# Optimization experiments

Measured on AMD Instinct MI355X. Metric: run time of the kernel, lower is better.

Reference implementation:

```python
import jax, jax.numpy as jnp
import numpy as np

N = 50000
E = 800000
IN_DIM = 128
EMB_DIM = 64
HID = 128
OUT_DIM = 64
VOCAB = 1000
NUM_GRAPHS = 128


def _gat(x, src, dst, W, a_s, a_d, b, n):
    # PyG GATConv, heads=1: h = x @ W (no bias); alpha_e = leaky_relu(a_s.h_src + a_d.h_dst, 0.2)
    h = x @ W                                  # [n, C]
    as_n = h @ a_s                             # [n]
    ad_n = h @ a_d                             # [n]
    logit = jax.nn.leaky_relu(as_n[src] + ad_n[dst], negative_slope=0.2)  # [E']
    # segment softmax over destination node
    m = jax.ops.segment_max(logit, dst, num_segments=n)
    e = jnp.exp(logit - m[dst])
    s = jax.ops.segment_sum(e, dst, num_segments=n)
    coef = e / s[dst]                          # [E']
    out = jax.ops.segment_sum(h[src] * coef[:, None], dst, num_segments=n)
    return out + b


def setup_inputs() -> dict:
    key = jax.random.key(0)
    ks = jax.random.split(key, 20)
    inp = {
        "x": jax.random.normal(ks[0], (N, IN_DIM), dtype=jnp.float32),
        "node_index": jax.random.randint(ks[1], (N,), 0, VOCAB),
        "edge_index": jax.random.randint(ks[2], (2, E), 0, N),
        "batch": jnp.sort(jax.random.randint(ks[3], (N,), 0, NUM_GRAPHS)),
        "emb": jax.random.normal(ks[4], (VOCAB, EMB_DIM), dtype=jnp.float32) * 0.1,
        "W1": jax.random.normal(ks[5], (IN_DIM + EMB_DIM, HID), dtype=jnp.float32) * 0.05,
        "a1s": jax.random.normal(ks[6], (HID,), dtype=jnp.float32) * 0.1,
        "a1d": jax.random.normal(ks[7], (HID,), dtype=jnp.float32) * 0.1,
        "b1": jnp.zeros((HID,), dtype=jnp.float32),
        "W2": jax.random.normal(ks[8], (HID, HID), dtype=jnp.float32) * 0.05,
        "a2s": jax.random.normal(ks[9], (HID,), dtype=jnp.float32) * 0.1,
        "a2d": jax.random.normal(ks[10], (HID,), dtype=jnp.float32) * 0.1,
        "b2": jnp.zeros((HID,), dtype=jnp.float32),
        "W3": jax.random.normal(ks[11], (HID, HID), dtype=jnp.float32) * 0.05,
        "a3s": jax.random.normal(ks[12], (HID,), dtype=jnp.float32) * 0.1,
        "a3d": jax.random.normal(ks[13], (HID,), dtype=jnp.float32) * 0.1,
        "b3": jnp.zeros((HID,), dtype=jnp.float32),
        "fcW": jax.random.normal(ks[14], (HID, OUT_DIM), dtype=jnp.float32) * 0.05,
        "fcb": jnp.zeros((OUT_DIM,), dtype=jnp.float32),
    }
    return inp


def reference(x, node_index, edge_index, batch, emb, W1, a1s, a1d, b1,
              W2, a2s, a2d, b2, W3, a3s, a3d, b3, fcW, fcb):
    n = x.shape[0]
    # embedding lookup + L2 normalize features, then concat
    ev = emb[node_index]                       # [N, EMB_DIM]
    norms = jnp.linalg.norm(x, axis=1, keepdims=True)
    norms = jnp.where(norms == 0, 1e-8, norms)
    h = jnp.concatenate([x / norms, ev], axis=1)  # [N, IN+EMB]
    # add self loops (PyG GATConv default add_self_loops=True)
    loop = jnp.arange(n)
    src = jnp.concatenate([edge_index[0], loop])
    dst = jnp.concatenate([edge_index[1], loop])
    h = jax.nn.gelu(_gat(h, src, dst, W1, a1s, a1d, b1, n))
    h = jax.nn.gelu(_gat(h, src, dst, W2, a2s, a2d, b2, n))
    h = jax.nn.gelu(_gat(h, src, dst, W3, a3s, a3d, b3, n))
    # global_add_pool over graphs
    g = jax.ops.segment_sum(h, batch, num_segments=NUM_GRAPHS)  # [G, HID]
    out = g @ fcW + fcb
    return jax.nn.leaky_relu(out, negative_slope=0.01)
```

## Files before the change

### kernel.cpp

```cpp
#include <hip/hip_runtime.h>

#define N_NODES 50000
#define N_EDGES 800000
#define IN_DIM 128
#define EMB_DIM 64
#define HID 128
#define OUT_DIM 64
#define NUM_GRAPHS 128
#define E_TOT (N_EDGES + N_NODES)
#define K1 (IN_DIM + EMB_DIM)
#define NB 391
#define EPT 16
#define EPB (256 * EPT)
#define PREPA_BLOCKS 12500
#define BHIST_BLOCKS 512

typedef __attribute__((ext_vector_type(8))) short bf16x8;
typedef __attribute__((ext_vector_type(4))) float f32x4;

__device__ __forceinline__ float gelu_f(float x) {
    float x3 = x * x * x;
    return 0.5f * x * (1.0f + tanhf(0.7978845608028654f * (x + 0.044715f * x3)));
}
__device__ __forceinline__ float lrelu02(float x) { return x > 0.f ? x : 0.2f * x; }
__device__ __forceinline__ float rl_f(float v, int j) {
    return __int_as_float(__builtin_amdgcn_readlane(__float_as_int(v), j));
}
__device__ __forceinline__ unsigned short f2bf(float f) {
    unsigned u = __float_as_uint(f);
    unsigned r = (u + 0x7fffu + ((u >> 16) & 1u)) >> 16;
    return (unsigned short)r;
}
__device__ __forceinline__ unsigned pk2bf(float a, float b) {
    return (unsigned)f2bf(a) | ((unsigned)f2bf(b) << 16);
}

__global__ __launch_bounds__(128) void k_prepW3(const float* __restrict__ W1, unsigned short* __restrict__ Wt1,
                                                const float* __restrict__ W2, unsigned short* __restrict__ Wt2,
                                                const float* __restrict__ W3, unsigned short* __restrict__ Wt3,
                                                int* __restrict__ bcnt, int* __restrict__ bfill) {
    int b = blockIdx.x;
    int c = threadIdx.x;
    if (b == K1 + 2 * HID) {
        for (int i = c; i < NB; i += 128) { bcnt[i] = 0; bfill[i] = 0; }
        return;
    }
    if (b < K1) {
        Wt1[(size_t)c * (K1 + 8) + b] = f2bf(W1[(size_t)b * HID + c]);
    } else if (b < K1 + HID) {
        int k = b - K1;
        Wt2[(size_t)c * (HID + 8) + k] = f2bf(W2[(size_t)k * HID + c]);
    } else {
        int k = b - K1 - HID;
        Wt3[(size_t)c * (HID + 8) + k] = f2bf(W3[(size_t)k * HID + c]);
    }
}

__global__ __launch_bounds__(256) void k_prepA_bhist(const float* __restrict__ x, const int* __restrict__ nidx,
                                                     const float* __restrict__ emb, unsigned* __restrict__ Abu,
                                                     const int* __restrict__ dst, int* __restrict__ bcnt) {
    __shared__ int h[NB];
    if (blockIdx.x >= PREPA_BLOCKS) {
        int nb = blockIdx.x - PREPA_BLOCKS;
        for (int i = threadIdx.x; i < NB; i += 256) h[i] = 0;
        __syncthreads();
        for (int e = nb * 256 + threadIdx.x; e < N_EDGES; e += BHIST_BLOCKS * 256)
            atomicAdd(&h[dst[e] >> 7], 1);
        __syncthreads();
        for (int i = threadIdx.x; i < NB; i += 256)
            if (h[i]) atomicAdd(&bcnt[i], h[i]);
        return;
    }
    int lane = threadIdx.x & 63;
    int node = (blockIdx.x * 256 + threadIdx.x) >> 6;
    if (node >= N_NODES) return;
    float2 v = ((const float2*)(x + (size_t)node * IN_DIM))[lane];
    float ss = v.x * v.x + v.y * v.y;
#pragma unroll
    for (int o = 32; o; o >>= 1) ss += __shfl_xor(ss, o);
    float nrm = sqrtf(ss);
    if (nrm == 0.f) nrm = 1e-8f;
    float inv = 1.f / nrm;
    unsigned* row = Abu + (size_t)node * (K1 / 2);
    row[lane] = pk2bf(v.x * inv, v.y * inv);
    int nid = __builtin_amdgcn_readfirstlane(nidx[node]);
    if (lane < 32) {
        float2 e = ((const float2*)(emb + (size_t)nid * EMB_DIM))[lane];
        row[64 + lane] = pk2bf(e.x, e.y);
    }
}

__global__ __launch_bounds__(512) void k_bscan(const int* __restrict__ bcnt, int* __restrict__ boff,
                                               int* __restrict__ rowptr) {
    __shared__ int sh[512];
    int t = threadIdx.x;
    int v = (t < NB) ? bcnt[t] : 0;
    sh[t] = v;
    __syncthreads();
    for (int o = 1; o < 512; o <<= 1) {
        int u = (t >= o) ? sh[t - o] : 0;
        __syncthreads();
        sh[t] += u;
        __syncthreads();
    }
    if (t < NB) boff[t] = sh[t] - v;
    if (t == NB - 1) boff[NB] = sh[t];
    if (t == 0) rowptr[N_NODES] = E_TOT;
}

__global__ __launch_bounds__(256) void k_passA(const int* __restrict__ src, const int* __restrict__ dst,
                                               const int* __restrict__ boff, int* __restrict__ bfill,
                                               unsigned* __restrict__ barr) {
    __shared__ int h[NB];
    __shared__ int base[NB];
    for (int i = threadIdx.x; i < NB; i += 256) h[i] = 0;
    __syncthreads();
    int e0 = blockIdx.x * EPB;
    int tag[EPT];
#pragma unroll
    for (int i = 0; i < EPT; i++) {
        int e = e0 + i * 256 + threadIdx.x;
        tag[i] = -1;
        if (e < N_EDGES) {
            int b = dst[e] >> 7;
            int r = atomicAdd(&h[b], 1);
            tag[i] = (b << 12) | r;
        }
    }
    __syncthreads();
    for (int i = threadIdx.x; i < NB; i += 256)
        base[i] = h[i] ? atomicAdd(&bfill[i], h[i]) : 0;
    __syncthreads();
#pragma unroll
    for (int i = 0; i < EPT; i++) {
        if (tag[i] >= 0) {
            int e = e0 + i * 256 + threadIdx.x;
            int b = tag[i] >> 12, r = tag[i] & 0xfff;
            unsigned s = (unsigned)src[e];
            unsigned dl = (unsigned)(dst[e] & 127);
            barr[boff[b] + base[b] + r] = s | (dl << 16);
        }
    }
}

__global__ __launch_bounds__(256) void k_passB(const unsigned* __restrict__ barr, const int* __restrict__ boff,
                                               int* __restrict__ rowptr, int* __restrict__ csr) {
    __shared__ int dcnt[128];
    __shared__ int dsum[128];
    __shared__ int locOff[128];
    int b = blockIdx.x;
    int t = threadIdx.x;
    int n0 = b << 7;
    int cnt = min(128, N_NODES - n0);
    int eb = boff[b], ee = boff[b + 1];
    if (t < 128) dcnt[t] = 0;
    __syncthreads();
    for (int i = eb + t; i < ee; i += 256) atomicAdd(&dcnt[barr[i] >> 16], 1);
    __syncthreads();
    int v = 0;
    if (t < 128) {
        v = (t < cnt) ? dcnt[t] + 1 : 0;
        dsum[t] = v;
    }
    __syncthreads();
    for (int o = 1; o < 128; o <<= 1) {
        int u = (t >= o && t < 128) ? dsum[t - o] : 0;
        __syncthreads();
        if (t < 128) dsum[t] += u;
        __syncthreads();
    }
    int csrBase = eb + n0;
    if (t < 128) {
        locOff[t] = dsum[t] - v;
        dcnt[t] = 0;
    }
    if (t < cnt) {
        int loc = dsum[t] - v;
        rowptr[n0 + t] = csrBase + loc;
        csr[csrBase + loc] = n0 + t;
    }
    __syncthreads();
    for (int i = eb + t; i < ee; i += 256) {
        unsigned vv = barr[i];
        int dl = vv >> 16;
        int s = (int)(vv & 0xffffu);
        int k = atomicAdd(&dcnt[dl], 1);
        csr[csrBase + locOff[dl] + 1 + k] = s;
    }
}

template <int K>
__global__ __launch_bounds__(256) void k_mgemm(const unsigned short* __restrict__ Abf,
                                               const unsigned short* __restrict__ WtP,
                                               const float* __restrict__ a_s, const float* __restrict__ a_d,
                                               unsigned short* __restrict__ Hbf,
                                               float* __restrict__ asn, float* __restrict__ adn) {
    constexpr int KP = K + 8;
    constexpr int NK = K / 32;
    __shared__ __align__(16) unsigned short Wl[128 * KP];
    {
        const uint4* gsrc = (const uint4*)WtP;
        uint4* ldst = (uint4*)Wl;
        const int nchunk = 128 * KP * 2 / 16;
        for (int i = threadIdx.x; i < nchunk; i += 256) ldst[i] = gsrc[i];
    }
    int lane = threadIdx.x & 63;
    int wv = threadIdx.x >> 6;
    int rowbase = blockIdx.x * 64 + wv * 16;
    if (rowbase >= N_NODES) { __syncthreads(); return; }
    int l15 = lane & 15, quad = lane >> 4;

    const unsigned short* Abase = Abf + (size_t)(rowbase + l15) * K + quad * 8;
    bf16x8 afr[NK];
#pragma unroll
    for (int i = 0; i < NK; i++) afr[i] = *(const bf16x8*)(Abase + i * 32);

    __syncthreads();

    f32x4 acc[8];
#pragma unroll
    for (int t = 0; t < 8; t++) acc[t] = (f32x4){0.f, 0.f, 0.f, 0.f};
#pragma unroll
    for (int i = 0; i < NK; i++) {
#pragma unroll
        for (int t = 0; t < 8; t++) {
            bf16x8 bf = *(const bf16x8*)(&Wl[(t * 16 + l15) * KP + i * 32 + quad * 8]);
            acc[t] = __builtin_amdgcn_mfma_f32_16x16x32_bf16(afr[i], bf, acc[t], 0, 0, 0);
        }
    }
    float asc[8], adc[8];
#pragma unroll
    for (int t = 0; t < 8; t++) { asc[t] = a_s[t * 16 + l15]; adc[t] = a_d[t * 16 + l15]; }
#pragma unroll
    for (int r = 0; r < 4; r++) {
        int row = rowbase + quad * 4 + r;
        float ps = 0.f, pd = 0.f;
#pragma unroll
        for (int t = 0; t < 8; t++) {
            float v = acc[t][r];
            Hbf[(size_t)row * HID + t * 16 + l15] = f2bf(v);
            ps = fmaf(v, asc[t], ps);
            pd = fmaf(v, adc[t], pd);
        }
#pragma unroll
        for (int o = 1; o < 16; o <<= 1) {
            ps += __shfl_xor(ps, o);
            pd += __shfl_xor(pd, o);
        }
        if (l15 == 0) { asn[row] = ps; adn[row] = pd; }
    }
}

template <bool OUT32>
__global__ __launch_bounds__(256) void k_aggr(const int* __restrict__ rowptr, const int* __restrict__ csr,
                                              const float* __restrict__ asn, const float* __restrict__ adn,
                                              const unsigned short* __restrict__ hbf,
                                              const float* __restrict__ bias, void* __restrict__ outp) {
    __shared__ float sh_e[4][64];
    __shared__ int sh_s[4][64];
    int lane = threadIdx.x & 63;
    int w = threadIdx.x >> 6;
    int node = blockIdx.x * 4 + w;
    if (node >= N_NODES) return;
    int st = rowptr[node], en = rowptr[node + 1];
    int deg = en - st;
    float ad = adn[node];

    if (deg <= 64) {
        int s = 0;
        float l = -1e30f;
        if (lane < deg) {
            s = csr[st + lane];
            l = lrelu02(asn[s] + ad);
        }
        float m = l;
#pragma unroll
        for (int o = 32; o; o >>= 1) m = fmaxf(m, __shfl_xor(m, o));
        float e = (lane < deg) ? __expf(l - m) : 0.f;
        float ssum = e;
#pragma unroll
        for (int o = 32; o; o >>= 1) ssum += __shfl_xor(ssum, o);
        float coef = e / ssum;

        const uint2* hu2 = (const uint2*)hbf;
        int half = lane >> 5, li = lane & 31;
        float4 acc = make_float4(0.f, 0.f, 0.f, 0.f);
        int j = 0;
        for (; j + 16 <= deg; j += 16) {
            int sx[8];
            float cf[8];
            uint2 vv[8];
#pragma unroll
            for (int q = 0; q < 8; q++) {
                int ii = j + 2 * q + half;
                sx[q] = __shfl(s, ii);
                cf[q] = __shfl(coef, ii);
            }
#pragma unroll
            for (int q = 0; q < 8; q++) vv[q] = hu2[(size_t)sx[q] * 32 + li];
#pragma unroll
            for (int q = 0; q < 8; q++) {
                acc.x = fmaf(cf[q], __int_as_float(vv[q].x << 16), acc.x);
                acc.y = fmaf(cf[q], __int_as_float(vv[q].x & 0xffff0000u), acc.y);
                acc.z = fmaf(cf[q], __int_as_float(vv[q].y << 16), acc.z);
                acc.w = fmaf(cf[q], __int_as_float(vv[q].y & 0xffff0000u), acc.w);
            }
        }
        for (; j + 8 <= deg; j += 8) {
            int sx[4];
            float cf[4];
            uint2 vv[4];
#pragma unroll
            for (int q = 0; q < 4; q++) {
                int ii = j + 2 * q + half;
                sx[q] = __shfl(s, ii);
                cf[q] = __shfl(coef, ii);
            }
#pragma unroll
            for (int q = 0; q < 4; q++) vv[q] = hu2[(size_t)sx[q] * 32 + li];
#pragma unroll
            for (int q = 0; q < 4; q++) {
                acc.x = fmaf(cf[q], __int_as_float(vv[q].x << 16), acc.x);
                acc.y = fmaf(cf[q], __int_as_float(vv[q].x & 0xffff0000u), acc.y);
                acc.z = fmaf(cf[q], __int_as_float(vv[q].y << 16), acc.z);
                acc.w = fmaf(cf[q], __int_as_float(vv[q].y & 0xffff0000u), acc.w);
            }
        }
        for (; j < deg; j += 2) {
            int ii = j + half;
            int ok = ii < deg;
            int ic = ok ? ii : j;
            int sx = __shfl(s, ic);
            float cf = __shfl(coef, ic);
            if (!ok) cf = 0.f;
            uint2 v = hu2[(size_t)sx * 32 + li];
            acc.x = fmaf(cf, __int_as_float(v.x << 16), acc.x);
            acc.y = fmaf(cf, __int_as_float(v.x & 0xffff0000u), acc.y);
            acc.z = fmaf(cf, __int_as_float(v.y << 16), acc.z);
            acc.w = fmaf(cf, __int_as_float(v.y & 0xffff0000u), acc.w);
        }
        acc.x += __shfl_xor(acc.x, 32);
        acc.y += __shfl_xor(acc.y, 32);
        acc.z += __shfl_xor(acc.z, 32);
        acc.w += __shfl_xor(acc.w, 32);
        float4 bb = ((const float4*)bias)[li];
        float r0 = gelu_f(acc.x + bb.x);
        float r1 = gelu_f(acc.y + bb.y);
        float r2 = gelu_f(acc.z + bb.z);
        float r3 = gelu_f(acc.w + bb.w);
        if (half == 0) {
            if constexpr (OUT32) {
                ((float4*)outp)[(size_t)node * 32 + li] = make_float4(r0, r1, r2, r3);
            } else {
                uint2 o;
                o.x = pk2bf(r0, r1);
                o.y = pk2bf(r2, r3);
                ((uint2*)outp)[(size_t)node * 32 + li] = o;
            }
        }
    } else {
        const unsigned* hu = (const unsigned*)hbf;
        float2 acc = make_float2(0.f, 0.f);
        float m = -1e30f;
        for (int i = st + lane; i < en; i += 64) {
            float l = lrelu02(asn[csr[i]] + ad);
            m = fmaxf(m, l);
        }
#pragma unroll
        for (int o = 32; o; o >>= 1) m = fmaxf(m, __shfl_xor(m, o));
        float ssum = 0.f;
        for (int i = st + lane; i < en; i += 64) {
            float l = lrelu02(asn[csr[i]] + ad);
            ssum += __expf(l - m);
        }
#pragma unroll
        for (int o = 32; o; o >>= 1) ssum += __shfl_xor(ssum, o);
        float inv = 1.f / ssum;
        for (int base = st; base < en; base += 64) {
            int cnt = min(64, en - base);
            if (lane < cnt) {
                int sx = csr[base + lane];
                float l = lrelu02(asn[sx] + ad);
                sh_e[w][lane] = __expf(l - m) * inv;
                sh_s[w][lane] = sx;
            }
            for (int j = 0; j < cnt; j++) {
                float c = sh_e[w][j];
                int sx = sh_s[w][j];
                unsigned v0 = hu[(size_t)sx * 64 + lane];
                acc.x = fmaf(c, __int_as_float(v0 << 16), acc.x);
                acc.y = fmaf(c, __int_as_float(v0 & 0xffff0000u), acc.y);
            }
        }
        float2 b = ((const float2*)bias)[lane];
        float rx = gelu_f(acc.x + b.x);
        float ry = gelu_f(acc.y + b.y);
        if constexpr (OUT32) {
            ((float2*)outp)[(size_t)node * 64 + lane] = make_float2(rx, ry);
        } else {
            ((unsigned*)outp)[(size_t)node * 64 + lane] = pk2bf(rx, ry);
        }
    }
}

__global__ __launch_bounds__(256) void k_poolfc(const float* __restrict__ h, const int* __restrict__ batch,
                                                const float* __restrict__ fcW, const float* __restrict__ fcb,
                                                float* __restrict__ out) {
    __shared__ float gv[HID];
    __shared__ float tmp[256];
    int g = blockIdx.x;
    int st, en;
    {
        int lo = 0, hi = N_NODES;
        while (lo < hi) { int mid = (lo + hi) >> 1; if (batch[mid] < g) lo = mid + 1; else hi = mid; }
        st = lo;
        lo = st; hi = N_NODES;
        while (lo < hi) { int mid = (lo + hi) >> 1; if (batch[mid] < g + 1) lo = mid + 1; else hi = mid; }
        en = lo;
    }
    int c = threadIdx.x & 127;
    int half = threadIdx.x >> 7;
    float acc = 0.f;
#pragma unroll 4
    for (int n = st + half; n < en; n += 2) acc += h[(size_t)n * HID + c];
    tmp[threadIdx.x] = acc;
    __syncthreads();
    if (threadIdx.x < HID) gv[threadIdx.x] = tmp[threadIdx.x] + tmp[threadIdx.x + 128];
    __syncthreads();
    if (threadIdx.x < OUT_DIM) {
        float a = fcb[threadIdx.x];
#pragma unroll 4
        for (int k = 0; k < HID; k++) a = fmaf(gv[k], fcW[k * OUT_DIM + threadIdx.x], a);
        out[g * OUT_DIM + threadIdx.x] = a > 0.f ? a : 0.01f * a;
    }
}

extern "C" void kernel_launch(void* const* d_in, const int* in_sizes, int n_in,
                              void* d_out, int out_size, void* d_ws, size_t ws_size,
                              hipStream_t stream) {
    const float* x    = (const float*)d_in[0];
    const int* nidx   = (const int*)d_in[1];
    const int* ei     = (const int*)d_in[2];
    const int* batch  = (const int*)d_in[3];
    const float* emb  = (const float*)d_in[4];
    const float* W1   = (const float*)d_in[5];
    const float* a1s  = (const float*)d_in[6];
    const float* a1d  = (const float*)d_in[7];
    const float* b1   = (const float*)d_in[8];
    const float* W2   = (const float*)d_in[9];
    const float* a2s  = (const float*)d_in[10];
    const float* a2d  = (const float*)d_in[11];
    const float* b2   = (const float*)d_in[12];
    const float* W3   = (const float*)d_in[13];
    const float* a3s  = (const float*)d_in[14];
    const float* a3d  = (const float*)d_in[15];
    const float* b3   = (const float*)d_in[16];
    const float* fcW  = (const float*)d_in[17];
    const float* fcb  = (const float*)d_in[18];
    float* out = (float*)d_out;
    const int* srcA = ei;
    const int* dstA = ei + N_EDGES;

    char* w = (char*)d_ws;
    auto alloc = [&](size_t bytes) -> char* {
        char* p = w;
        w += (bytes + 511) & ~(size_t)511;
        return p;
    };
    char* region0 = alloc((size_t)N_NODES * HID * 4);
    unsigned* Abu = (unsigned*)region0;
    float* h3f    = (float*)region0;
    unsigned short* hLin = (unsigned short*)alloc((size_t)N_NODES * HID * 2);
    unsigned short* hAct = (unsigned short*)alloc((size_t)N_NODES * HID * 2);
    float* asn   = (float*)alloc((size_t)N_NODES * 4);
    float* adn   = (float*)alloc((size_t)N_NODES * 4);
    int* rowptr  = (int*)alloc((size_t)(N_NODES + 1) * 4);
    int* bcnt    = (int*)alloc((size_t)NB * 4);
    int* boff    = (int*)alloc((size_t)(NB + 1) * 4);
    int* bfill   = (int*)alloc((size_t)NB * 4);
    unsigned* barr = (unsigned*)alloc((size_t)N_EDGES * 4);
    int* csr     = (int*)alloc((size_t)E_TOT * 4);
    unsigned short* Wt1 = (unsigned short*)alloc((size_t)HID * (K1 + 8) * 2);
    unsigned short* Wt2 = (unsigned short*)alloc((size_t)HID * (HID + 8) * 2);
    unsigned short* Wt3 = (unsigned short*)alloc((size_t)HID * (HID + 8) * 2);

    k_prepW3<<<K1 + 2 * HID + 1, 128, 0, stream>>>(W1, Wt1, W2, Wt2, W3, Wt3, bcnt, bfill);
    k_prepA_bhist<<<PREPA_BLOCKS + BHIST_BLOCKS, 256, 0, stream>>>(x, nidx, emb, Abu, dstA, bcnt);

    k_bscan<<<1, 512, 0, stream>>>(bcnt, boff, rowptr);
    k_passA<<<(N_EDGES + EPB - 1) / EPB, 256, 0, stream>>>(srcA, dstA, boff, bfill, barr);
    k_passB<<<NB, 256, 0, stream>>>(barr, boff, rowptr, csr);

    int gemmBlocks = (N_NODES + 63) / 64;
    int aggrBlocks = (N_NODES + 3) / 4;

    k_mgemm<K1><<<gemmBlocks, 256, 0, stream>>>((const unsigned short*)Abu, Wt1, a1s, a1d, hLin, asn, adn);
    k_aggr<false><<<aggrBlocks, 256, 0, stream>>>(rowptr, csr, asn, adn, hLin, b1, hAct);
    k_mgemm<HID><<<gemmBlocks, 256, 0, stream>>>(hAct, Wt2, a2s, a2d, hLin, asn, adn);
    k_aggr<false><<<aggrBlocks, 256, 0, stream>>>(rowptr, csr, asn, adn, hLin, b2, hAct);
    k_mgemm<HID><<<gemmBlocks, 256, 0, stream>>>(hAct, Wt3, a3s, a3d, hLin, asn, adn);
    k_aggr<true><<<aggrBlocks, 256, 0, stream>>>(rowptr, csr, asn, adn, hLin, b3, h3f);

    k_poolfc<<<NUM_GRAPHS, 256, 0, stream>>>(h3f, batch, fcW, fcb, out);
}
```

Measured before the change: 339.1 us.

## Halve GEMM weight LDS footprint and prefetch neighbor rows before softmax in aggregation

```diff
diff --git a/kernel.cpp b/kernel.cpp
--- a/kernel.cpp
+++ b/kernel.cpp
@@ -23,9 +23,6 @@
     return 0.5f * x * (1.0f + tanhf(0.7978845608028654f * (x + 0.044715f * x3)));
 }
 __device__ __forceinline__ float lrelu02(float x) { return x > 0.f ? x : 0.2f * x; }
-__device__ __forceinline__ float rl_f(float v, int j) {
-    return __int_as_float(__builtin_amdgcn_readlane(__float_as_int(v), j));
-}
 __device__ __forceinline__ unsigned short f2bf(float f) {
     unsigned u = __float_as_uint(f);
     unsigned r = (u + 0x7fffu + ((u >> 16) & 1u)) >> 16;
@@ -197,24 +194,23 @@
                                                float* __restrict__ asn, float* __restrict__ adn) {
     constexpr int KP = K + 8;
     constexpr int NK = K / 32;
-    __shared__ __align__(16) unsigned short Wl[128 * KP];
-    {
-        const uint4* gsrc = (const uint4*)WtP;
-        uint4* ldst = (uint4*)Wl;
-        const int nchunk = 128 * KP * 2 / 16;
-        for (int i = threadIdx.x; i < nchunk; i += 256) ldst[i] = gsrc[i];
-    }
+    constexpr int HCH = 64 * KP * 2 / 16;
+    __shared__ __align__(16) unsigned short Wl[64 * KP];
     int lane = threadIdx.x & 63;
     int wv = threadIdx.x >> 6;
     int rowbase = blockIdx.x * 64 + wv * 16;
-    if (rowbase >= N_NODES) { __syncthreads(); return; }
+    bool active = rowbase < N_NODES;
     int l15 = lane & 15, quad = lane >> 4;
 
-    const unsigned short* Abase = Abf + (size_t)(rowbase + l15) * K + quad * 8;
+    int arow = active ? (rowbase + l15) : 0;
+    const unsigned short* Abase = Abf + (size_t)arow * K + quad * 8;
     bf16x8 afr[NK];
 #pragma unroll
     for (int i = 0; i < NK; i++) afr[i] = *(const bf16x8*)(Abase + i * 32);
 
+    const uint4* gsrc = (const uint4*)WtP;
+    uint4* ldst = (uint4*)Wl;
+    for (int i = threadIdx.x; i < HCH; i += 256) ldst[i] = gsrc[i];
     __syncthreads();
 
     f32x4 acc[8];
@@ -223,11 +219,23 @@
 #pragma unroll
     for (int i = 0; i < NK; i++) {
 #pragma unroll
-        for (int t = 0; t < 8; t++) {
+        for (int t = 0; t < 4; t++) {
             bf16x8 bf = *(const bf16x8*)(&Wl[(t * 16 + l15) * KP + i * 32 + quad * 8]);
             acc[t] = __builtin_amdgcn_mfma_f32_16x16x32_bf16(afr[i], bf, acc[t], 0, 0, 0);
         }
     }
+    __syncthreads();
+    for (int i = threadIdx.x; i < HCH; i += 256) ldst[i] = gsrc[i + HCH];
+    __syncthreads();
+#pragma unroll
+    for (int i = 0; i < NK; i++) {
+#pragma unroll
+        for (int t = 4; t < 8; t++) {
+            bf16x8 bf = *(const bf16x8*)(&Wl[((t - 4) * 16 + l15) * KP + i * 32 + quad * 8]);
+            acc[t] = __builtin_amdgcn_mfma_f32_16x16x32_bf16(afr[i], bf, acc[t], 0, 0, 0);
+        }
+    }
+    if (!active) return;
     float asc[8], adc[8];
 #pragma unroll
     for (int t = 0; t < 8; t++) { asc[t] = a_s[t * 16 + l15]; adc[t] = a_d[t * 16 + l15]; }
@@ -264,29 +272,80 @@
     if (node >= N_NODES) return;
     int st = rowptr[node], en = rowptr[node + 1];
     int deg = en - st;
+    int degU = __builtin_amdgcn_readfirstlane(deg);
     float ad = adn[node];
-
-    if (deg <= 64) {
+    const uint2* hu2 = (const uint2*)hbf;
+    int half = lane >> 5, li = lane & 31;
+
+    if (degU <= 32) {
+        int s = 0;
+        if (lane < degU) s = csr[st + lane];
+        uint2 vv[16];
+#pragma unroll
+        for (int q = 0; q < 16; q++) {
+            if (2 * q < degU) {
+                int sx = __shfl(s, 2 * q + half);
+                vv[q] = hu2[(size_t)sx * 32 + li];
+            }
+        }
+        float l = -1e30f;
+        if (lane < degU) l = lrelu02(asn[s] + ad);
+        float m = l;
+#pragma unroll
+        for (int o = 32; o; o >>= 1) m = fmaxf(m, __shfl_xor(m, o));
+        float e = (lane < degU) ? __expf(l - m) : 0.f;
+        float ssum = e;
+#pragma unroll
+        for (int o = 32; o; o >>= 1) ssum += __shfl_xor(ssum, o);
+        float coef = e / ssum;
+        float4 acc = make_float4(0.f, 0.f, 0.f, 0.f);
+#pragma unroll
+        for (int q = 0; q < 16; q++) {
+            if (2 * q < degU) {
+                float cf = __shfl(coef, 2 * q + half);
+                acc.x = fmaf(cf, __int_as_float(vv[q].x << 16), acc.x);
+                acc.y = fmaf(cf, __int_as_float(vv[q].x & 0xffff0000u), acc.y);
+                acc.z = fmaf(cf, __int_as_float(vv[q].y << 16), acc.z);
+                acc.w = fmaf(cf, __int_as_float(vv[q].y & 0xffff0000u), acc.w);
+            }
+        }
+        acc.x += __shfl_xor(acc.x, 32);
+        acc.y += __shfl_xor(acc.y, 32);
+        acc.z += __shfl_xor(acc.z, 32);
+        acc.w += __shfl_xor(acc.w, 32);
+        float4 bb = ((const float4*)bias)[li];
+        float r0 = gelu_f(acc.x + bb.x);
+        float r1 = gelu_f(acc.y + bb.y);
+        float r2 = gelu_f(acc.z + bb.z);
+        float r3 = gelu_f(acc.w + bb.w);
+        if (half == 0) {
+            if constexpr (OUT32) {
+                ((float4*)outp)[(size_t)node * 32 + li] = make_float4(r0, r1, r2, r3);
+            } else {
+                uint2 o;
+                o.x = pk2bf(r0, r1);
+                o.y = pk2bf(r2, r3);
+                ((uint2*)outp)[(size_t)node * 32 + li] = o;
+            }
+        }
+    } else if (degU <= 64) {
         int s = 0;
         float l = -1e30f;
-        if (lane < deg) {
+        if (lane < degU) {
             s = csr[st + lane];
             l = lrelu02(asn[s] + ad);
         }
         float m = l;
 #pragma unroll
         for (int o = 32; o; o >>= 1) m = fmaxf(m, __shfl_xor(m, o));
-        float e = (lane < deg) ? __expf(l - m) : 0.f;
+        float e = (lane < degU) ? __expf(l - m) : 0.f;
         float ssum = e;
 #pragma unroll
         for (int o = 32; o; o >>= 1) ssum += __shfl_xor(ssum, o);
         float coef = e / ssum;
-
-        const uint2* hu2 = (const uint2*)hbf;
-        int half = lane >> 5, li = lane & 31;
         float4 acc = make_float4(0.f, 0.f, 0.f, 0.f);
         int j = 0;
-        for (; j + 16 <= deg; j += 16) {
+        for (; j + 16 <= degU; j += 16) {
             int sx[8];
             float cf[8];
             uint2 vv[8];
@@ -306,33 +365,12 @@
                 acc.w = fmaf(cf[q], __int_as_float(vv[q].y & 0xffff0000u), acc.w);
             }
         }
-        for (; j + 8 <= deg; j += 8) {
-            int sx[4];
-            float cf[4];
-            uint2 vv[4];
-#pragma unroll
-            for (int q = 0; q < 4; q++) {
-                int ii = j + 2 * q + half;
-                sx[q] = __shfl(s, ii);
-                cf[q] = __shfl(coef, ii);
-            }
-#pragma unroll
-            for (int q = 0; q < 4; q++) vv[q] = hu2[(size_t)sx[q] * 32 + li];
-#pragma unroll
-            for (int q = 0; q < 4; q++) {
-                acc.x = fmaf(cf[q], __int_as_float(vv[q].x << 16), acc.x);
-                acc.y = fmaf(cf[q], __int_as_float(vv[q].x & 0xffff0000u), acc.y);
-                acc.z = fmaf(cf[q], __int_as_float(vv[q].y << 16), acc.z);
-                acc.w = fmaf(cf[q], __int_as_float(vv[q].y & 0xffff0000u), acc.w);
-            }
-        }
-        for (; j < deg; j += 2) {
+        for (; j < degU; j += 2) {
             int ii = j + half;
-            int ok = ii < deg;
-            int ic = ok ? ii : j;
+            int ic = (ii < degU) ? ii : j;
             int sx = __shfl(s, ic);
             float cf = __shfl(coef, ic);
-            if (!ok) cf = 0.f;
+            if (ii >= degU) cf = 0.f;
             uint2 v = hu2[(size_t)sx * 32 + li];
             acc.x = fmaf(cf, __int_as_float(v.x << 16), acc.x);
             acc.y = fmaf(cf, __int_as_float(v.x & 0xffff0000u), acc.y);
```

New measurement: 374.1 us. 1.1x slower.

## Stage CSR bucket scatters in LDS and widen buckets to 256 nodes

Applied to the files above, without the earlier changes.

```diff
diff --git a/kernel.cpp b/kernel.cpp
--- a/kernel.cpp
+++ b/kernel.cpp
@@ -9,11 +9,14 @@
 #define NUM_GRAPHS 128
 #define E_TOT (N_EDGES + N_NODES)
 #define K1 (IN_DIM + EMB_DIM)
-#define NB 391
+#define BSH 8
+#define BNODES 256
+#define NB 196
 #define EPT 16
 #define EPB (256 * EPT)
 #define PREPA_BLOCKS 12500
 #define BHIST_BLOCKS 512
+#define PB_CAP 5376
 
 typedef __attribute__((ext_vector_type(8))) short bf16x8;
 typedef __attribute__((ext_vector_type(4))) float f32x4;
@@ -23,9 +26,6 @@
     return 0.5f * x * (1.0f + tanhf(0.7978845608028654f * (x + 0.044715f * x3)));
 }
 __device__ __forceinline__ float lrelu02(float x) { return x > 0.f ? x : 0.2f * x; }
-__device__ __forceinline__ float rl_f(float v, int j) {
-    return __int_as_float(__builtin_amdgcn_readlane(__float_as_int(v), j));
-}
 __device__ __forceinline__ unsigned short f2bf(float f) {
     unsigned u = __float_as_uint(f);
     unsigned r = (u + 0x7fffu + ((u >> 16) & 1u)) >> 16;
@@ -65,7 +65,7 @@
         for (int i = threadIdx.x; i < NB; i += 256) h[i] = 0;
         __syncthreads();
         for (int e = nb * 256 + threadIdx.x; e < N_EDGES; e += BHIST_BLOCKS * 256)
-            atomicAdd(&h[dst[e] >> 7], 1);
+            atomicAdd(&h[dst[e] >> BSH], 1);
         __syncthreads();
         for (int i = threadIdx.x; i < NB; i += 256)
             if (h[i]) atomicAdd(&bcnt[i], h[i]);
@@ -112,80 +112,110 @@
                                                const int* __restrict__ boff, int* __restrict__ bfill,
                                                unsigned* __restrict__ barr) {
     __shared__ int h[NB];
-    __shared__ int base[NB];
-    for (int i = threadIdx.x; i < NB; i += 256) h[i] = 0;
+    __shared__ int hbase[NB];
+    __shared__ int lofs[NB];
+    __shared__ int ssc[256];
+    __shared__ unsigned val[EPB];
+    __shared__ unsigned char bid[EPB];
+    int t = threadIdx.x;
+    for (int i = t; i < NB; i += 256) h[i] = 0;
     __syncthreads();
     int e0 = blockIdx.x * EPB;
     int tag[EPT];
 #pragma unroll
     for (int i = 0; i < EPT; i++) {
-        int e = e0 + i * 256 + threadIdx.x;
+        int e = e0 + i * 256 + t;
         tag[i] = -1;
         if (e < N_EDGES) {
-            int b = dst[e] >> 7;
+            int b = dst[e] >> BSH;
             int r = atomicAdd(&h[b], 1);
             tag[i] = (b << 12) | r;
         }
     }
     __syncthreads();
-    for (int i = threadIdx.x; i < NB; i += 256)
-        base[i] = h[i] ? atomicAdd(&bfill[i], h[i]) : 0;
-    __syncthreads();
+    int v = (t < NB) ? h[t] : 0;
+    ssc[t] = v;
+    __syncthreads();
+    for (int o = 1; o < 256; o <<= 1) {
+        int u = (t >= o) ? ssc[t - o] : 0;
+        __syncthreads();
+        ssc[t] += u;
+        __syncthreads();
+    }
+    if (t < NB) {
+        lofs[t] = ssc[t] - v;
+        hbase[t] = v ? atomicAdd(&bfill[t], v) : 0;
+    }
+    __syncthreads();
+    int tot = ssc[255];
 #pragma unroll
     for (int i = 0; i < EPT; i++) {
         if (tag[i] >= 0) {
-            int e = e0 + i * 256 + threadIdx.x;
+            int e = e0 + i * 256 + t;
             int b = tag[i] >> 12, r = tag[i] & 0xfff;
             unsigned s = (unsigned)src[e];
-            unsigned dl = (unsigned)(dst[e] & 127);
-            barr[boff[b] + base[b] + r] = s | (dl << 16);
-        }
+            unsigned dl = (unsigned)(dst[e] & (BNODES - 1));
+            int idx = lofs[b] + r;
+            val[idx] = s | (dl << 16);
+            bid[idx] = (unsigned char)b;
+        }
+    }
+    __syncthreads();
+    for (int i = t; i < tot; i += 256) {
+        int b = bid[i];
+        barr[boff[b] + hbase[b] + (i - lofs[b])] = val[i];
     }
 }
 
 __global__ __launch_bounds__(256) void k_passB(const unsigned* __restrict__ barr, const int* __restrict__ boff,
                                                int* __restrict__ rowptr, int* __restrict__ csr) {
-    __shared__ int dcnt[128];
-    __shared__ int dsum[128];
-    __shared__ int locOff[128];
+    __shared__ int dcnt[256];
+    __shared__ int dsum[256];
+    __shared__ int locOff[256];
+    __shared__ unsigned stg[PB_CAP];
     int b = blockIdx.x;
     int t = threadIdx.x;
-    int n0 = b << 7;
-    int cnt = min(128, N_NODES - n0);
+    int n0 = b << BSH;
+    int cnt = min(BNODES, N_NODES - n0);
     int eb = boff[b], ee = boff[b + 1];
-    if (t < 128) dcnt[t] = 0;
+    int ne = ee - eb;
+    dcnt[t] = 0;
     __syncthreads();
     for (int i = eb + t; i < ee; i += 256) atomicAdd(&dcnt[barr[i] >> 16], 1);
     __syncthreads();
-    int v = 0;
-    if (t < 128) {
-        v = (t < cnt) ? dcnt[t] + 1 : 0;
-        dsum[t] = v;
-    }
-    __syncthreads();
-    for (int o = 1; o < 128; o <<= 1) {
-        int u = (t >= o && t < 128) ? dsum[t - o] : 0;
-        __syncthreads();
-        if (t < 128) dsum[t] += u;
+    int v = (t < cnt) ? dcnt[t] + 1 : 0;
+    dsum[t] = v;
+    __syncthreads();
+    for (int o = 1; o < 256; o <<= 1) {
+        int u = (t >= o) ? dsum[t - o] : 0;
+        __syncthreads();
+        dsum[t] += u;
         __syncthreads();
     }
     int csrBase = eb + n0;
-    if (t < 128) {
-        locOff[t] = dsum[t] - v;
-        dcnt[t] = 0;
-    }
-    if (t < cnt) {
-        int loc = dsum[t] - v;
-        rowptr[n0 + t] = csrBase + loc;
-        csr[csrBase + loc] = n0 + t;
-    }
-    __syncthreads();
-    for (int i = eb + t; i < ee; i += 256) {
-        unsigned vv = barr[i];
-        int dl = vv >> 16;
-        int s = (int)(vv & 0xffffu);
-        int k = atomicAdd(&dcnt[dl], 1);
-        csr[csrBase + locOff[dl] + 1 + k] = s;
+    locOff[t] = dsum[t] - v;
+    dcnt[t] = 0;
+    if (t < cnt) rowptr[n0 + t] = csrBase + locOff[t];
+    int total = ne + cnt;
+    __syncthreads();
+    if (total <= PB_CAP) {
+        if (t < cnt) stg[locOff[t]] = (unsigned)(n0 + t);
+        for (int i = eb + t; i < ee; i += 256) {
+            unsigned vv = barr[i];
+            int dl = vv >> 16;
+            int k = atomicAdd(&dcnt[dl], 1);
+            stg[locOff[dl] + 1 + k] = vv & 0xffffu;
+        }
+        __syncthreads();
+        for (int i = t; i < total; i += 256) csr[csrBase + i] = (int)stg[i];
+    } else {
+        if (t < cnt) csr[csrBase + locOff[t]] = n0 + t;
+        for (int i = eb + t; i < ee; i += 256) {
+            unsigned vv = barr[i];
+            int dl = vv >> 16;
+            int k = atomicAdd(&dcnt[dl], 1);
+            csr[csrBase + locOff[dl] + 1 + k] = (int)(vv & 0xffffu);
+        }
     }
 }
 
```

Measured after the change: 339.7 us. Within noise of the previous version (+0.2%).
